# Kernel optimization log

Hardware: AMD Instinct MI355X
Metric: run time of the kernel (lower is better)

The kernel has to match this reference:

```python
import jax, jax.numpy as jnp
import numpy as np

B, M, K, E, V, HOPS = 256, 128, 4, 512, 32000, 3


def setup_inputs() -> dict:
    key = jax.random.key(0)
    ks = jax.random.split(key, 12)

    def emb_table(k):
        t = 0.1 * jax.random.normal(k, (V, E), dtype=jnp.float32)
        return t.at[0].set(0.0)  # padding_idx=0

    inp = {
        "context": jax.random.randint(ks[0], (B, M, K), 0, V),
        "y_": jax.random.randint(ks[1], (B,), 0, V),
        "h_": jax.random.normal(ks[2], (1, B, E), dtype=jnp.float32),
        # embedding tables; C[i] tied to A[i+1], so distinct: A0,A1,A2,C2
        "A0": emb_table(ks[3]),
        "A1": emb_table(ks[4]),
        "A2": emb_table(ks[5]),
        "C2": emb_table(ks[6]),
        # GRU (single layer, single step): PyTorch layout [3E, E] and [3E]
        "W_ih": 0.05 * jax.random.normal(ks[7], (3 * E, E), dtype=jnp.float32),
        "W_hh": 0.05 * jax.random.normal(ks[8], (3 * E, E), dtype=jnp.float32),
        "b_ih": jnp.zeros((3 * E,), dtype=jnp.float32),
        "b_hh": jnp.zeros((3 * E,), dtype=jnp.float32),
        # lin_vocab: Linear(2E -> V)
        "lin_W": 0.02 * jax.random.normal(ks[9], (V, 2 * E), dtype=jnp.float32),
        "lin_b": jnp.zeros((V,), dtype=jnp.float32),
    }
    return inp


def _gru_step(x, h, W_ih, W_hh, b_ih, b_hh):
    gi = x @ W_ih.T + b_ih  # [B, 3E]
    gh = h @ W_hh.T + b_hh
    i_r, i_z, i_n = jnp.split(gi, 3, axis=-1)
    h_r, h_z, h_n = jnp.split(gh, 3, axis=-1)
    r = jax.nn.sigmoid(i_r + h_r)
    z = jax.nn.sigmoid(i_z + h_z)
    n = jnp.tanh(i_n + r * h_n)
    return (1.0 - z) * n + z * h


def reference(context, y_, h_, A0, A1, A2, C2, W_ih, W_hh, b_ih, b_hh, lin_W, lin_b):
    # memories[hop] = sum_k A[hop][context], memories[hops] = sum_k C[hops-1][context]
    tables = [A0, A1, A2, C2]
    memories = [t[context].sum(axis=2) for t in tables]  # each [B, M, E]

    m = A1[y_]  # C[0](y_) -- C[0].weight tied to A[1].weight, [B, E]
    h = _gru_step(m, h_[0], W_ih, W_hh, b_ih, b_hh)  # [B, E]

    q = h
    p = None
    p_vocab = None
    for hop in range(HOPS):
        p = jnp.einsum("bme,be->bm", memories[hop], q)  # dot-attention scores
        attn = jax.nn.softmax(p, axis=1)
        o = jnp.einsum("bm,bme->be", attn, memories[hop + 1])
        if hop == 0:
            p_vocab = jnp.concatenate([q, o], axis=1) @ lin_W.T + lin_b  # [B, V]
        q = q + o

    p_ptr = p  # last hop's pre-softmax scores [B, M]
    return (p_ptr, p_vocab, h[None])  # h: [1, B, E]
```

## Files before the change

### kernel.cpp

```cpp
#include <hip/hip_runtime.h>
#include <hip/hip_bf16.h>
#include <stdint.h>
#include <stddef.h>

#define Bb 256
#define Mm 128
#define Ee 512
#define Vv 32000
#define E3 1536

typedef __attribute__((ext_vector_type(8))) short bf16x8;
typedef __attribute__((ext_vector_type(4))) float f32x4;

__device__ __forceinline__ float bf2f(unsigned short u) {
  union { unsigned int i; float f; } v; v.i = ((unsigned int)u) << 16; return v.f;
}
__device__ __forceinline__ unsigned int f2bf(float f) {
  union { float f; unsigned int u; } v; v.f = f;
  unsigned int u = v.u;
  return ((u + 0x7fffu + ((u >> 16) & 1u)) >> 16);
}

__global__ void convert_kernel(const float* __restrict__ A0, const float* __restrict__ A1,
                               const float* __restrict__ A2,
                               unsigned short* __restrict__ tabB) {
  const int t = blockIdx.y;
  const float* src = (t == 0) ? A0 : (t == 1) ? A1 : A2;
  unsigned short* dst = tabB + (size_t)t * Vv * Ee;
  const int n4 = Vv * Ee / 4;
  for (int i = blockIdx.x * blockDim.x + threadIdx.x; i < n4; i += gridDim.x * blockDim.x) {
    f32x4 v = __builtin_nontemporal_load((const f32x4*)src + i);
    unsigned int o0 = f2bf(v.x) | (f2bf(v.y) << 16);
    unsigned int o1 = f2bf(v.z) | (f2bf(v.w) << 16);
    ((uint2*)dst)[i] = make_uint2(o0, o1);
  }
}

__global__ void gru_gemm_kernel(const int* __restrict__ y,
                                const float* __restrict__ A1,
                                const float* __restrict__ hprev,
                                const float* __restrict__ W_ih,
                                const float* __restrict__ W_hh,
                                float* __restrict__ gi,
                                float* __restrict__ gh) {
  const int z = blockIdx.z;
  const float* W = z ? W_hh : W_ih;
  float* C = z ? gh : gi;
  const int by = blockIdx.x * 64;
  const int jy = blockIdx.y * 64;
  __shared__ float As[16][65];
  __shared__ float Bs[16][65];
  const int tx = threadIdx.x & 15, ty = threadIdx.x >> 4;
  float acc[4][4] = {};
  for (int k0 = 0; k0 < Ee; k0 += 16) {
#pragma unroll
    for (int it = 0; it < 4; ++it) {
      int r = ty + it * 16;
      int row = by + r;
      const float* arow = z ? (hprev + (size_t)row * Ee) : (A1 + (size_t)y[row] * Ee);
      As[tx][r] = arow[k0 + tx];
      Bs[tx][r] = W[(size_t)(jy + r) * Ee + k0 + tx];
    }
    __syncthreads();
#pragma unroll
    for (int kk = 0; kk < 16; ++kk) {
      float a[4], bb[4];
#pragma unroll
      for (int i = 0; i < 4; ++i) { a[i] = As[kk][ty * 4 + i]; bb[i] = Bs[kk][tx * 4 + i]; }
#pragma unroll
      for (int i = 0; i < 4; ++i)
#pragma unroll
        for (int j = 0; j < 4; ++j)
          acc[i][j] += a[i] * bb[j];
    }
    __syncthreads();
  }
#pragma unroll
  for (int i = 0; i < 4; ++i)
#pragma unroll
    for (int j = 0; j < 4; ++j)
      C[(size_t)(by + ty * 4 + i) * E3 + jy + tx * 4 + j] = acc[i][j];
}

__global__ __launch_bounds__(1024) void fused_kernel(
    const int* __restrict__ ctx,
    const unsigned short* __restrict__ tabB,
    const float* __restrict__ A0, const float* __restrict__ A1,
    const float* __restrict__ A2,
    const float* __restrict__ gi, const float* __restrict__ gh,
    const float* __restrict__ b_ih, const float* __restrict__ b_hh,
    const float* __restrict__ h0,
    float* __restrict__ out_h, unsigned short* __restrict__ in2,
    float* __restrict__ p_out) {
  extern __shared__ char smem[];
  unsigned short* Vlds = (unsigned short*)smem;
  float* p_lds = (float*)(smem + 131072);
  float* qbuf = (float*)(smem + 131584);
  float* obuf = (float*)(smem + 133632);

  const int b = blockIdx.x;
  const int tid = threadIdx.x;
  const int lane = tid & 63, w = tid >> 6;

  if (tid < 512) {
    const int e = tid;
    const float* gib = gi + (size_t)b * E3;
    const float* ghb = gh + (size_t)b * E3;
    float ir = gib[e] + b_ih[e];
    float iz = gib[512 + e] + b_ih[512 + e];
    float inn = gib[1024 + e] + b_ih[1024 + e];
    float hr = ghb[e] + b_hh[e];
    float hz = ghb[512 + e] + b_hh[512 + e];
    float hn = ghb[1024 + e] + b_hh[1024 + e];
    float r = 1.f / (1.f + __expf(-(ir + hr)));
    float z = 1.f / (1.f + __expf(-(iz + hz)));
    float n = tanhf(inn + r * hn);
    float hp = h0[(size_t)b * Ee + e];
    float hnew = (1.f - z) * n + z * hp;
    out_h[(size_t)b * Ee + e] = hnew;
    in2[(size_t)b * 1024 + e] = (unsigned short)f2bf(hnew);
    qbuf[e] = hnew;
  }

#define GATHER_B(T)                                                          \
  {                                                                          \
    const unsigned short* Tb = tabB + (size_t)(T) * ((size_t)Vv * Ee);       \
    _Pragma("unroll 2")                                                      \
    for (int r8 = 0; r8 < 8; ++r8) {                                         \
      const int row = w * 8 + r8;                                            \
      const int4 cc = *(const int4*)(ctx + ((size_t)b * Mm + row) * 4);      \
      uint4 va = *(const uint4*)(Tb + (size_t)cc.x * Ee + lane * 8);         \
      uint4 vb = *(const uint4*)(Tb + (size_t)cc.y * Ee + lane * 8);         \
      uint4 vc = *(const uint4*)(Tb + (size_t)cc.z * Ee + lane * 8);         \
      uint4 vd = *(const uint4*)(Tb + (size_t)cc.w * Ee + lane * 8);         \
      const unsigned int* pa = (const unsigned int*)&va;                     \
      const unsigned int* pb = (const unsigned int*)&vb;                     \
      const unsigned int* pc = (const unsigned int*)&vc;                     \
      const unsigned int* pd = (const unsigned int*)&vd;                     \
      unsigned int o[4];                                                     \
      _Pragma("unroll")                                                      \
      for (int j = 0; j < 4; ++j) {                                          \
        float lo = bf2f((unsigned short)(pa[j] & 0xffff)) +                  \
                   bf2f((unsigned short)(pb[j] & 0xffff)) +                  \
                   bf2f((unsigned short)(pc[j] & 0xffff)) +                  \
                   bf2f((unsigned short)(pd[j] & 0xffff));                   \
        float hi = bf2f((unsigned short)(pa[j] >> 16)) +                     \
                   bf2f((unsigned short)(pb[j] >> 16)) +                     \
                   bf2f((unsigned short)(pc[j] >> 16)) +                     \
                   bf2f((unsigned short)(pd[j] >> 16));                      \
        o[j] = f2bf(lo) | (f2bf(hi) << 16);                                  \
      }                                                                      \
      *(uint4*)(Vlds + (size_t)row * Ee + lane * 8) = *(uint4*)o;            \
    }                                                                        \
  }

#define GATHER_F(TAB)                                                        \
  {                                                                          \
    _Pragma("unroll 2")                                                      \
    for (int r8 = 0; r8 < 8; ++r8) {                                         \
      const int row = w * 8 + r8;                                            \
      const int4 cc = *(const int4*)(ctx + ((size_t)b * Mm + row) * 4);      \
      const float* s0 = TAB + (size_t)cc.x * Ee + lane * 8;                  \
      const float* s1 = TAB + (size_t)cc.y * Ee + lane * 8;                  \
      const float* s2 = TAB + (size_t)cc.z * Ee + lane * 8;                  \
      const float* s3 = TAB + (size_t)cc.w * Ee + lane * 8;                  \
      float4 a0 = *(const float4*)s0, a1 = *(const float4*)(s0 + 4);         \
      float4 b0 = *(const float4*)s1, b1 = *(const float4*)(s1 + 4);         \
      float4 c0 = *(const float4*)s2, c1 = *(const float4*)(s2 + 4);         \
      float4 d0 = *(const float4*)s3, d1 = *(const float4*)(s3 + 4);         \
      unsigned int o[4];                                                     \
      o[0] = f2bf(a0.x + b0.x + c0.x + d0.x) |                               \
             (f2bf(a0.y + b0.y + c0.y + d0.y) << 16);                        \
      o[1] = f2bf(a0.z + b0.z + c0.z + d0.z) |                               \
             (f2bf(a0.w + b0.w + c0.w + d0.w) << 16);                        \
      o[2] = f2bf(a1.x + b1.x + c1.x + d1.x) |                               \
             (f2bf(a1.y + b1.y + c1.y + d1.y) << 16);                        \
      o[3] = f2bf(a1.z + b1.z + c1.z + d1.z) |                               \
             (f2bf(a1.w + b1.w + c1.w + d1.w) << 16);                        \
      *(uint4*)(Vlds + (size_t)row * Ee + lane * 8) = *(uint4*)o;            \
    }                                                                        \
  }

#define GATHER(T, TAB) { if (tabB) GATHER_B(T) else GATHER_F(TAB) }

#define SCORE_PHASE(EMIT)                                                    \
  {                                                                          \
    float qf[8];                                                             \
    *(float4*)&qf[0] = *(const float4*)&qbuf[lane * 8];                      \
    *(float4*)&qf[4] = *(const float4*)&qbuf[lane * 8 + 4];                  \
    _Pragma("unroll")                                                        \
    for (int r = 0; r < 8; ++r) {                                            \
      const int m = w * 8 + r;                                               \
      uint4 kv = *(const uint4*)(Vlds + (size_t)m * Ee + lane * 8);          \
      const unsigned int* p4 = (const unsigned int*)&kv;                     \
      float s = 0.f;                                                         \
      _Pragma("unroll")                                                      \
      for (int x = 0; x < 4; ++x) {                                          \
        s += bf2f((unsigned short)(p4[x] & 0xffff)) * qf[2 * x];             \
        s += bf2f((unsigned short)(p4[x] >> 16)) * qf[2 * x + 1];            \
      }                                                                      \
      _Pragma("unroll")                                                      \
      for (int off = 32; off > 0; off >>= 1) s += __shfl_down(s, off);       \
      if (lane == 0) { EMIT; }                                               \
    }                                                                        \
  }

#define SOFTMAX_PHASE                                                        \
  if (tid < 64) {                                                            \
    float v0 = p_lds[tid], v1 = p_lds[tid + 64];                             \
    float mx = fmaxf(v0, v1);                                                \
    _Pragma("unroll")                                                        \
    for (int off = 32; off > 0; off >>= 1) mx = fmaxf(mx, __shfl_xor(mx, off)); \
    float e0 = __expf(v0 - mx), e1 = __expf(v1 - mx);                        \
    float s = e0 + e1;                                                       \
    _Pragma("unroll")                                                        \
    for (int off = 32; off > 0; off >>= 1) s += __shfl_xor(s, off);          \
    float inv = 1.f / s;                                                     \
    p_lds[tid] = e0 * inv;                                                   \
    p_lds[tid + 64] = e1 * inv;                                              \
  }

#define O_PHASE                                                              \
  {                                                                          \
    const int g = tid >> 8, t = tid & 255;                                   \
    const int e2 = t * 2;                                                    \
    float a0 = 0.f, a1 = 0.f;                                                \
    _Pragma("unroll 4")                                                      \
    for (int m = g * 32; m < g * 32 + 32; ++m) {                             \
      unsigned int vv = *(const unsigned int*)(Vlds + (size_t)m * Ee + e2);  \
      float ww = p_lds[m];                                                   \
      a0 += ww * bf2f((unsigned short)(vv & 0xffff));                        \
      a1 += ww * bf2f((unsigned short)(vv >> 16));                           \
    }                                                                        \
    obuf[g * 512 + e2] = a0;                                                 \
    obuf[g * 512 + e2 + 1] = a1;                                             \
  }

  GATHER(0, A0)
  __syncthreads();
  SCORE_PHASE(p_lds[m] = s)
  __syncthreads();
  SOFTMAX_PHASE
  GATHER(1, A1)
  __syncthreads();
  O_PHASE
  __syncthreads();
  if (tid < 512) {
    const int e = tid;
    float o = obuf[e] + obuf[512 + e] + obuf[1024 + e] + obuf[1536 + e];
    qbuf[e] = qbuf[e] + o;
    in2[(size_t)b * 1024 + 512 + e] = (unsigned short)f2bf(o);
  }
  __syncthreads();

  SCORE_PHASE(p_lds[m] = s)
  __syncthreads();
  SOFTMAX_PHASE
  GATHER(2, A2)
  __syncthreads();
  O_PHASE
  __syncthreads();
  if (tid < 512) {
    const int e = tid;
    qbuf[e] = qbuf[e] + obuf[e] + obuf[512 + e] + obuf[1024 + e] + obuf[1536 + e];
  }
  __syncthreads();

  SCORE_PHASE(p_out[b * Mm + m] = s)
}

__global__ __launch_bounds__(512) void pvocab_kernel(
    const unsigned short* __restrict__ in2,
    const float* __restrict__ lin_W,
    const float* __restrict__ lin_b,
    float* __restrict__ out_pv) {
  const int v0 = blockIdx.x * 128;
  const int tid = threadIdx.x;
  const int lane = tid & 63, w = tid >> 6;
  const int wm = w >> 2, wn = w & 3;
  const int l15 = lane & 15, lg = lane >> 4;
  __shared__ __align__(16) unsigned short As[256][72];
  __shared__ __align__(16) unsigned short Ws[128][72];

  f32x4 acc[8][2];
#pragma unroll
  for (int i = 0; i < 8; ++i)
#pragma unroll
    for (int j = 0; j < 2; ++j)
      acc[i][j] = (f32x4){0.f, 0.f, 0.f, 0.f};

  for (int k0 = 0; k0 < 1024; k0 += 64) {
    {
      const int c = tid & 7, r0 = tid >> 3;
#pragma unroll
      for (int it = 0; it < 4; ++it) {
        int r = r0 + it * 64;
        *(uint4*)(&As[r][c * 8]) = *(const uint4*)(in2 + (size_t)r * 1024 + k0 + c * 8);
      }
    }
    {
      const int c = tid & 15, r0 = tid >> 4;
#pragma unroll
      for (int it = 0; it < 4; ++it) {
        int r = r0 + it * 32;
        float4 wv = *(const float4*)(lin_W + (size_t)(v0 + r) * 1024 + k0 + c * 4);
        unsigned int u0 = f2bf(wv.x) | (f2bf(wv.y) << 16);
        unsigned int u1 = f2bf(wv.z) | (f2bf(wv.w) << 16);
        *(uint2*)(&Ws[r][c * 4]) = make_uint2(u0, u1);
      }
    }
    __syncthreads();
#pragma unroll
    for (int kk = 0; kk < 2; ++kk) {
      bf16x8 wf[2];
#pragma unroll
      for (int j = 0; j < 2; ++j)
        wf[j] = *(const bf16x8*)(&Ws[wn * 32 + j * 16 + l15][kk * 32 + lg * 8]);
#pragma unroll
      for (int i = 0; i < 8; ++i) {
        bf16x8 af = *(const bf16x8*)(&As[wm * 128 + i * 16 + l15][kk * 32 + lg * 8]);
#pragma unroll
        for (int j = 0; j < 2; ++j)
          acc[i][j] = __builtin_amdgcn_mfma_f32_16x16x32_bf16(af, wf[j], acc[i][j], 0, 0, 0);
      }
    }
    __syncthreads();
  }

#pragma unroll
  for (int j = 0; j < 2; ++j) {
    int v = v0 + wn * 32 + j * 16 + l15;
    float bias = lin_b[v];
#pragma unroll
    for (int i = 0; i < 8; ++i) {
      int brow = wm * 128 + i * 16 + lg * 4;
#pragma unroll
      for (int rr = 0; rr < 4; ++rr)
        out_pv[(size_t)(brow + rr) * Vv + v] = acc[i][j][rr] + bias;
    }
  }
}

extern "C" void kernel_launch(void* const* d_in, const int* in_sizes, int n_in,
                              void* d_out, int out_size, void* d_ws, size_t ws_size,
                              hipStream_t stream) {
  const int* ctx = (const int*)d_in[0];
  const int* y = (const int*)d_in[1];
  const float* h0 = (const float*)d_in[2];
  const float* A0 = (const float*)d_in[3];
  const float* A1 = (const float*)d_in[4];
  const float* A2 = (const float*)d_in[5];
  const float* W_ih = (const float*)d_in[7];
  const float* W_hh = (const float*)d_in[8];
  const float* b_ih = (const float*)d_in[9];
  const float* b_hh = (const float*)d_in[10];
  const float* lin_W = (const float*)d_in[11];
  const float* lin_b = (const float*)d_in[12];

  const size_t tabBytes = (size_t)3 * Vv * Ee * 2;
  const size_t giBytes = (size_t)Bb * E3 * 4;
  const size_t in2Bytes = (size_t)Bb * 1024 * 2;
  const bool bf16path = ws_size >= tabBytes + 2 * giBytes + in2Bytes;

  char* ws = (char*)d_ws;
  size_t off = 0;
  unsigned short* tabB = nullptr;
  if (bf16path) { tabB = (unsigned short*)ws; off += tabBytes; }
  float* gi = (float*)(ws + off); off += giBytes;
  float* gh = (float*)(ws + off); off += giBytes;
  unsigned short* in2 = (unsigned short*)(ws + off);

  float* out = (float*)d_out;
  float* p_ptr = out;
  float* p_voc = out + Bb * Mm;
  float* out_h = out + Bb * Mm + (size_t)Bb * Vv;

  if (bf16path)
    convert_kernel<<<dim3(4096, 3), 256, 0, stream>>>(A0, A1, A2, tabB);
  gru_gemm_kernel<<<dim3(4, 24, 2), 256, 0, stream>>>(y, A1, h0, W_ih, W_hh, gi, gh);
  hipFuncSetAttribute((const void*)fused_kernel,
                      hipFuncAttributeMaxDynamicSharedMemorySize, 141824);
  fused_kernel<<<Bb, 1024, 141824, stream>>>(ctx, tabB, A0, A1, A2, gi, gh,
                                             b_ih, b_hh, h0, out_h, in2, p_ptr);
  pvocab_kernel<<<Vv / 128, 512, 0, stream>>>(in2, lin_W, lin_b, p_voc);
}
```

Baseline: 239.5 us.

## Split vocab GEMM over batch halves and swizzle shared-memory tiles

Launches the vocab projection GEMM with a second grid dimension so each block computes 128 batch rows instead of 256. This doubles the block count and shrinks LDS and accumulator use for better occupancy and load balance. Shared-memory tiles drop padding in favour of an XOR-style column swizzle to avoid bank conflicts. The trade-off is that the fp32 lin_W weights are read and converted to bf16 twice.

```diff
diff --git a/kernel.cpp b/kernel.cpp
--- a/kernel.cpp
+++ b/kernel.cpp
@@ -275,54 +275,65 @@
     const float* __restrict__ lin_b,
     float* __restrict__ out_pv) {
   const int v0 = blockIdx.x * 128;
+  const int m0 = blockIdx.y * 128;
   const int tid = threadIdx.x;
   const int lane = tid & 63, w = tid >> 6;
   const int wm = w >> 2, wn = w & 3;
   const int l15 = lane & 15, lg = lane >> 4;
-  __shared__ __align__(16) unsigned short As[256][72];
-  __shared__ __align__(16) unsigned short Ws[128][72];
-
-  f32x4 acc[8][2];
-#pragma unroll
-  for (int i = 0; i < 8; ++i)
+  __shared__ __align__(16) unsigned short As[128][64];
+  __shared__ __align__(16) unsigned short Ws[128][64];
+
+  f32x4 acc[4][2];
+#pragma unroll
+  for (int i = 0; i < 4; ++i)
 #pragma unroll
     for (int j = 0; j < 2; ++j)
       acc[i][j] = (f32x4){0.f, 0.f, 0.f, 0.f};
 
   for (int k0 = 0; k0 < 1024; k0 += 64) {
     {
-      const int c = tid & 7, r0 = tid >> 3;
+      const int u = tid & 7;
+      const int rb = tid >> 3;
+#pragma unroll
+      for (int it = 0; it < 2; ++it) {
+        int r = rb + it * 64;
+        uint4 val = *(const uint4*)(in2 + (size_t)(m0 + r) * 1024 + k0 + u * 8);
+        *(uint4*)(&As[r][((u + r) & 7) * 8]) = val;
+      }
+    }
+    {
+      const int c = tid & 15;
+      const int rb = tid >> 4;
 #pragma unroll
       for (int it = 0; it < 4; ++it) {
-        int r = r0 + it * 64;
-        *(uint4*)(&As[r][c * 8]) = *(const uint4*)(in2 + (size_t)r * 1024 + k0 + c * 8);
+        int r = rb + it * 32;
+        float4 wv = *(const float4*)(lin_W + (size_t)(v0 + r) * 1024 + k0 + c * 4);
+        unsigned int o0 = f2bf(wv.x) | (f2bf(wv.y) << 16);
+        unsigned int o1 = f2bf(wv.z) | (f2bf(wv.w) << 16);
+        int u = c >> 1, h = c & 1;
+        *(uint2*)(&Ws[r][((u + r) & 7) * 8 + h * 4]) = make_uint2(o0, o1);
       }
     }
-    {
-      const int c = tid & 15, r0 = tid >> 4;
-#pragma unroll
-      for (int it = 0; it < 4; ++it) {
-        int r = r0 + it * 32;
-        float4 wv = *(const float4*)(lin_W + (size_t)(v0 + r) * 1024 + k0 + c * 4);
-        unsigned int u0 = f2bf(wv.x) | (f2bf(wv.y) << 16);
-        unsigned int u1 = f2bf(wv.z) | (f2bf(wv.w) << 16);
-        *(uint2*)(&Ws[r][c * 4]) = make_uint2(u0, u1);
+    __syncthreads();
+#pragma unroll
+    for (int kk = 0; kk < 2; ++kk) {
+      const int cu = kk * 4 + lg;
+      bf16x8 wf[2], af[4];
+#pragma unroll
+      for (int j = 0; j < 2; ++j) {
+        int row = wn * 32 + j * 16 + l15;
+        wf[j] = *(const bf16x8*)(&Ws[row][((cu + row) & 7) * 8]);
       }
-    }
-    __syncthreads();
-#pragma unroll
-    for (int kk = 0; kk < 2; ++kk) {
-      bf16x8 wf[2];
-#pragma unroll
-      for (int j = 0; j < 2; ++j)
-        wf[j] = *(const bf16x8*)(&Ws[wn * 32 + j * 16 + l15][kk * 32 + lg * 8]);
-#pragma unroll
-      for (int i = 0; i < 8; ++i) {
-        bf16x8 af = *(const bf16x8*)(&As[wm * 128 + i * 16 + l15][kk * 32 + lg * 8]);
+#pragma unroll
+      for (int i = 0; i < 4; ++i) {
+        int row = wm * 64 + i * 16 + l15;
+        af[i] = *(const bf16x8*)(&As[row][((cu + row) & 7) * 8]);
+      }
+#pragma unroll
+      for (int i = 0; i < 4; ++i)
 #pragma unroll
         for (int j = 0; j < 2; ++j)
-          acc[i][j] = __builtin_amdgcn_mfma_f32_16x16x32_bf16(af, wf[j], acc[i][j], 0, 0, 0);
-      }
+          acc[i][j] = __builtin_amdgcn_mfma_f32_16x16x32_bf16(af[i], wf[j], acc[i][j], 0, 0, 0);
     }
     __syncthreads();
   }
@@ -332,8 +343,8 @@
     int v = v0 + wn * 32 + j * 16 + l15;
     float bias = lin_b[v];
 #pragma unroll
-    for (int i = 0; i < 8; ++i) {
-      int brow = wm * 128 + i * 16 + lg * 4;
+    for (int i = 0; i < 4; ++i) {
+      int brow = m0 + wm * 64 + i * 16 + lg * 4;
 #pragma unroll
       for (int rr = 0; rr < 4; ++rr)
         out_pv[(size_t)(brow + rr) * Vv + v] = acc[i][j][rr] + bias;
@@ -382,5 +393,5 @@
                       hipFuncAttributeMaxDynamicSharedMemorySize, 141824);
   fused_kernel<<<Bb, 1024, 141824, stream>>>(ctx, tabB, A0, A1, A2, gi, gh,
                                              b_ih, b_hh, h0, out_h, in2, p_ptr);
-  pvocab_kernel<<<Vv / 128, 512, 0, stream>>>(in2, lin_W, lin_b, p_voc);
-}
+  pvocab_kernel<<<dim3(Vv / 128, 2), 512, 0, stream>>>(in2, lin_W, lin_b, p_voc);
+}
```

After: 231.0 us. -3.6%, faster.

## Drop LDS staging in vocab GEMM, load MFMA fragments directly from global

Applied to the files above, without the earlier changes.

The vocab-projection GEMM no longer stages A and W tiles through shared memory with barriers. Each wave now loads its bf16 activation fragments and fp32 weight fragments straight from global memory into registers, converting to bf16 on the fly. Block size doubles to 1024 threads (16 waves), and each wave handles 64 rows instead of 128, which cuts accumulator register use. This removes the LDS round trip and syncs, but W rows are now loaded redundantly by the four wm-waves that share them, and the global loads are narrower and less coalesced, leaning on L1/L2 to absorb the repeats.

```diff
diff --git a/kernel.cpp b/kernel.cpp
--- a/kernel.cpp
+++ b/kernel.cpp
@@ -269,71 +269,71 @@
   SCORE_PHASE(p_out[b * Mm + m] = s)
 }
 
-__global__ __launch_bounds__(512) void pvocab_kernel(
+__global__ __launch_bounds__(1024) void pvocab_kernel(
     const unsigned short* __restrict__ in2,
     const float* __restrict__ lin_W,
     const float* __restrict__ lin_b,
     float* __restrict__ out_pv) {
-  const int v0 = blockIdx.x * 128;
+  const int n0 = blockIdx.x * 128;
   const int tid = threadIdx.x;
   const int lane = tid & 63, w = tid >> 6;
   const int wm = w >> 2, wn = w & 3;
   const int l15 = lane & 15, lg = lane >> 4;
-  __shared__ __align__(16) unsigned short As[256][72];
-  __shared__ __align__(16) unsigned short Ws[128][72];
-
-  f32x4 acc[8][2];
-#pragma unroll
-  for (int i = 0; i < 8; ++i)
+  const int m_base = wm * 64;
+  const int n_base = n0 + wn * 32;
+
+  f32x4 acc[4][2];
+#pragma unroll
+  for (int i = 0; i < 4; ++i)
 #pragma unroll
     for (int j = 0; j < 2; ++j)
       acc[i][j] = (f32x4){0.f, 0.f, 0.f, 0.f};
 
+  const float* w0p = lin_W + (size_t)(n_base + l15) * 1024;
+  const float* w1p = lin_W + (size_t)(n_base + 16 + l15) * 1024;
+  const unsigned short* a0p = in2 + (size_t)(m_base + l15) * 1024;
+
   for (int k0 = 0; k0 < 1024; k0 += 64) {
-    {
-      const int c = tid & 7, r0 = tid >> 3;
-#pragma unroll
-      for (int it = 0; it < 4; ++it) {
-        int r = r0 + it * 64;
-        *(uint4*)(&As[r][c * 8]) = *(const uint4*)(in2 + (size_t)r * 1024 + k0 + c * 8);
+#pragma unroll
+    for (int kk = 0; kk < 2; ++kk) {
+      const int col = k0 + kk * 32 + lg * 8;
+      bf16x8 wf[2];
+      {
+        float4 lo = *(const float4*)(w0p + col);
+        float4 hi = *(const float4*)(w0p + col + 4);
+        unsigned int u[4];
+        u[0] = f2bf(lo.x) | (f2bf(lo.y) << 16);
+        u[1] = f2bf(lo.z) | (f2bf(lo.w) << 16);
+        u[2] = f2bf(hi.x) | (f2bf(hi.y) << 16);
+        u[3] = f2bf(hi.z) | (f2bf(hi.w) << 16);
+        wf[0] = *(bf16x8*)u;
+      }
+      {
+        float4 lo = *(const float4*)(w1p + col);
+        float4 hi = *(const float4*)(w1p + col + 4);
+        unsigned int u[4];
+        u[0] = f2bf(lo.x) | (f2bf(lo.y) << 16);
+        u[1] = f2bf(lo.z) | (f2bf(lo.w) << 16);
+        u[2] = f2bf(hi.x) | (f2bf(hi.y) << 16);
+        u[3] = f2bf(hi.z) | (f2bf(hi.w) << 16);
+        wf[1] = *(bf16x8*)u;
+      }
+#pragma unroll
+      for (int i = 0; i < 4; ++i) {
+        bf16x8 af = *(const bf16x8*)(a0p + (size_t)i * 16384 + col);
+        acc[i][0] = __builtin_amdgcn_mfma_f32_16x16x32_bf16(af, wf[0], acc[i][0], 0, 0, 0);
+        acc[i][1] = __builtin_amdgcn_mfma_f32_16x16x32_bf16(af, wf[1], acc[i][1], 0, 0, 0);
       }
     }
-    {
-      const int c = tid & 15, r0 = tid >> 4;
-#pragma unroll
-      for (int it = 0; it < 4; ++it) {
-        int r = r0 + it * 32;
-        float4 wv = *(const float4*)(lin_W + (size_t)(v0 + r) * 1024 + k0 + c * 4);
-        unsigned int u0 = f2bf(wv.x) | (f2bf(wv.y) << 16);
-        unsigned int u1 = f2bf(wv.z) | (f2bf(wv.w) << 16);
-        *(uint2*)(&Ws[r][c * 4]) = make_uint2(u0, u1);
-      }
-    }
-    __syncthreads();
-#pragma unroll
-    for (int kk = 0; kk < 2; ++kk) {
-      bf16x8 wf[2];
-#pragma unroll
-      for (int j = 0; j < 2; ++j)
-        wf[j] = *(const bf16x8*)(&Ws[wn * 32 + j * 16 + l15][kk * 32 + lg * 8]);
-#pragma unroll
-      for (int i = 0; i < 8; ++i) {
-        bf16x8 af = *(const bf16x8*)(&As[wm * 128 + i * 16 + l15][kk * 32 + lg * 8]);
-#pragma unroll
-        for (int j = 0; j < 2; ++j)
-          acc[i][j] = __builtin_amdgcn_mfma_f32_16x16x32_bf16(af, wf[j], acc[i][j], 0, 0, 0);
-      }
-    }
-    __syncthreads();
   }
 
 #pragma unroll
   for (int j = 0; j < 2; ++j) {
-    int v = v0 + wn * 32 + j * 16 + l15;
+    int v = n_base + j * 16 + l15;
     float bias = lin_b[v];
 #pragma unroll
-    for (int i = 0; i < 8; ++i) {
-      int brow = wm * 128 + i * 16 + lg * 4;
+    for (int i = 0; i < 4; ++i) {
+      int brow = m_base + i * 16 + lg * 4;
 #pragma unroll
       for (int rr = 0; rr < 4; ++rr)
         out_pv[(size_t)(brow + rr) * Vv + v] = acc[i][j][rr] + bias;
@@ -382,5 +382,5 @@
                       hipFuncAttributeMaxDynamicSharedMemorySize, 141824);
   fused_kernel<<<Bb, 1024, 141824, stream>>>(ctx, tabB, A0, A1, A2, gi, gh,
                                              b_ih, b_hh, h0, out_h, in2, p_ptr);
-  pvocab_kernel<<<Vv / 128, 512, 0, stream>>>(in2, lin_W, lin_b, p_voc);
-}
+  pvocab_kernel<<<Vv / 128, 1024, 0, stream>>>(in2, lin_W, lin_b, p_voc);
+}
```

Result: slower. 291.3 us (+21.6%).
